# Performance work log

Measured on AMD Instinct MI355X. Metric: run time of the kernel, lower is better.

The kernel has to match this reference:

```python
import jax, jax.numpy as jnp
import numpy as np

# dims: B batches, N points/batch, S sampled points/batch, M image-projected points/batch,
# V voxels, (H,Wd) range-image size, HID hidden size, NSC scales, NCLS classes
B, N, S, M, V, H, Wd, HID, NSC, NCLS = 2, 120000, 40000, 30000, 100000, 256, 1024, 128, 4, 20


def setup_inputs() -> dict:
    key = jax.random.key(0)
    ks = jax.random.split(key, 24)
    f = jnp.float32
    w = lambda k, shp: (0.02 * jax.random.normal(k, shp, f))
    rows = jax.random.randint(ks[10], (B, M), 0, H, jnp.int32)
    cols = jax.random.randint(ks[11], (B, M), 0, Wd, jnp.int32)
    return {
        "pts_feat_layers": jax.random.normal(ks[0], (NSC, V, HID), f),
        "pts_sample_feat": jax.random.normal(ks[1], (NSC, B * S, HID), f),
        "img_latent_full": jax.random.normal(ks[2], (B, HID, H, Wd), f),
        "img_feat_layers": jax.random.normal(ks[3], (NSC, B * M, HID), f),
        "leaner_W": w(ks[4], (NSC, HID, HID)), "leaner_b": jnp.zeros((NSC, HID), f),
        "fcs1_W": w(ks[5], (NSC, 2 * HID, HID)), "fcs1_b": jnp.zeros((NSC, HID), f),
        "fcs2_W": w(ks[6], (NSC, HID, HID)), "fcs2_b": jnp.zeros((NSC, HID), f),
        "cls_W1": w(ks[7], (NSC * HID, 128)), "cls_b1": jnp.zeros((128,), f),
        "cls_W2": w(ks[8], (128, NCLS)), "cls_b2": jnp.zeros((NCLS,), f),
        "points_img": jnp.stack([rows, cols], axis=-1),              # [B,M,2]
        "point2img_index": jax.random.randint(ks[12], (B, M), 0, N, jnp.int32),
        "sample_index": jax.random.randint(ks[13], (B, S), 0, N, jnp.int32),
        "coors_inv": jax.random.randint(ks[14], (B * N,), 0, V, jnp.int32),
    }


def reference(pts_feat_layers, pts_sample_feat, img_latent_full, img_feat_layers,
              leaner_W, leaner_b, fcs1_W, fcs1_b, fcs2_W, fcs2_b,
              cls_W1, cls_b1, cls_W2, cls_b2,
              points_img, point2img_index, sample_index, coors_inv):
    dt = img_latent_full.dtype
    img_hw = jnp.transpose(img_latent_full, (0, 2, 3, 1))  # [B,H,Wd,HID]
    bar = jnp.arange(B)[:, None]
    # gather image features at projected pixel coords: [B,M,HID]
    img_at_pts = img_hw[bar, points_img[:, :, 0], points_img[:, :, 1]]
    # scatter image features to per-point slots (pts_img_batch_new): [B,N,HID]
    pimg = jax.vmap(lambda idx, v: jnp.zeros((N, HID), dt).at[idx].set(v))(point2img_index, img_at_pts)

    fuse_feats, enc_feats = [], []
    for i in range(NSC):
        # p2img_mapping_spsample: output values depend only on sampled feats + image gather
        sf = pts_sample_feat[i].reshape(B, S, HID)
        sp = jax.vmap(lambda idx, v: jnp.zeros((N, HID), dt).at[idx].set(v))(sample_index, sf)
        sp = sp + pimg  # sample_point_feat == sample_point_feat_f  [B,N,HID]
        # scatter fused point features back into voxel features, then gather per point
        pts_feat = pts_feat_layers[i].at[coors_inv].set(sp.reshape(B * N, HID))
        pts_point = pts_feat[coors_inv].reshape(B, N, HID)
        # p2img_mapping: gather the image-projected points per batch  [B*M,HID]
        pts_g = jnp.take_along_axis(pts_point, point2img_index[:, :, None], axis=1).reshape(B * M, HID)
        fl = jax.nn.relu(pts_g @ leaner_W[i] + leaner_b[i])
        fc = jnp.concatenate([img_feat_layers[i], fl], axis=1) @ fcs1_W[i] + fcs1_b[i]
        fw = jax.nn.sigmoid(fc @ fcs2_W[i] + fcs2_b[i])
        fuse_feats.append(jax.nn.relu(fc * fw))
        enc_feats.append(sp.reshape(B * N, HID))

    seg = jnp.concatenate(fuse_feats, axis=1)                       # [B*M, NSC*HID]
    img_seg_logits = jax.nn.relu(seg @ cls_W1 + cls_b1) @ cls_W2 + cls_b2  # [B*M, NCLS]
    output_3d = jnp.concatenate(enc_feats, axis=1)                  # [B*N, NSC*HID]
    return img_seg_logits, output_3d
```

## Files before the change

kernel.cpp:

```cpp
#include <hip/hip_runtime.h>
#include <hip/hip_bf16.h>
#include <math.h>

#define B_    2
#define N_    120000
#define S_    40000
#define M_    30000
#define V_    100000
#define H_    256
#define WD_   1024
#define HID_  128
#define NSC_  4
#define NCLS_ 20
#define BM_   60000
#define BS_   80000
#define BN_   240000

#define SCALE_BLKS 3752
#define OUT3D_BLKS 30000

typedef __attribute__((ext_vector_type(8))) short bfrag8;
typedef __attribute__((ext_vector_type(4))) float facc4;
typedef __attribute__((ext_vector_type(4))) unsigned short usvec4;

__device__ __forceinline__ unsigned short f2bf(float f){
  unsigned u = __builtin_bit_cast(unsigned, f);
  u += 0x7fffu + ((u >> 16) & 1u);
  return (unsigned short)(u >> 16);
}
__device__ __forceinline__ float bf2f(unsigned short s){
  return __builtin_bit_cast(float, ((unsigned)s) << 16);
}

__global__ __launch_bounds__(256) void k_front(
    const float* __restrict__ img, const int* __restrict__ ptsimg,
    unsigned short* __restrict__ iap,
    const int* __restrict__ p2i, const int* __restrict__ si,
    const int* __restrict__ ci,
    int* __restrict__ win_p, int* __restrict__ win_s, int* __restrict__ win_c,
    const float* __restrict__ lW, const float* __restrict__ f1W,
    const float* __restrict__ f2W, const float* __restrict__ c1W,
    const float* __restrict__ c2W,
    unsigned short* __restrict__ lwT, unsigned short* __restrict__ f1T,
    unsigned short* __restrict__ f2T, unsigned short* __restrict__ c1T,
    unsigned short* __restrict__ c2T){
  int bid = blockIdx.x;
  if (bid < 30000){
    int t = bid * 256 + threadIdx.x;
    int row = t >> 7, h = t & 127;
    int b = row / M_;
    int r = ptsimg[row * 2 + 0];
    int c = ptsimg[row * 2 + 1];
    iap[t] = f2bf(img[(((size_t)b * HID_ + h) * H_ + r) * WD_ + c]);
    return;
  }
  if (bid < 30938){
    int t = (bid - 30000) * 256 + threadIdx.x;
    if (t < BM_) atomicMax(&win_p[(t / M_) * N_ + p2i[t]], t);
    if (t < BS_) atomicMax(&win_s[(t / S_) * N_ + si[t]], t);
    if (t < BN_) atomicMax(&win_c[ci[t]], t);
    return;
  }
  {
    int t = (bid - 30938) * 256 + threadIdx.x;
    if (t < 65536){
      int i = t >> 14, r = t & 16383, n = r >> 7, k = r & 127;
      lwT[i * 16384 + n * 128 + k] = f2bf(lW[i * 16384 + k * 128 + n]);
    } else if (t < 196608){
      int e = t - 65536;
      int i = e >> 15, r = e & 32767, n = r >> 8, k = r & 255;
      f1T[i * 32768 + n * 256 + k] = f2bf(f1W[i * 32768 + k * 128 + n]);
    } else if (t < 262144){
      int e = t - 196608;
      int i = e >> 14, r = e & 16383, n = r >> 7, k = r & 127;
      f2T[i * 16384 + n * 128 + k] = f2bf(f2W[i * 16384 + k * 128 + n]);
    } else if (t < 327680){
      int e = t - 262144;
      int n = e >> 9, k = e & 511;
      c1T[n * 512 + k] = f2bf(c1W[k * 128 + n]);
    } else if (t < 330240){
      int e = t - 327680;
      int n = e >> 7, k = e & 127;
      c2T[n * 128 + k] = f2bf(c2W[k * NCLS_ + n]);
    }
    return;
  }
}

__global__ __launch_bounds__(256, 3) void k_mega(
    const float* __restrict__ samp, const unsigned short* __restrict__ iap,
    const int* __restrict__ win_p, const int* __restrict__ win_s,
    const int* __restrict__ win_c, const int* __restrict__ p2i,
    const int* __restrict__ ci, const float* __restrict__ imgf,
    const unsigned short* __restrict__ lwT, const float* __restrict__ lb,
    const unsigned short* __restrict__ f1T, const float* __restrict__ f1b,
    const unsigned short* __restrict__ f2T, const float* __restrict__ f2b,
    unsigned short* __restrict__ seg, float* __restrict__ o3d){
  __shared__ char lds[49152];
  if (blockIdx.x >= SCALE_BLKS){
    int t = (blockIdx.x - SCALE_BLKS) * 256 + threadIdx.x;
    int j = t >> 5, q = t & 31;
    int sj = win_s[j], pj = win_p[j];
    facc4 iv = {0.f, 0.f, 0.f, 0.f};
    if (pj >= 0){
      usvec4 u = __builtin_nontemporal_load((const usvec4*)(iap + (size_t)pj * HID_ + q * 4));
      iv.x = bf2f(u.x); iv.y = bf2f(u.y); iv.z = bf2f(u.z); iv.w = bf2f(u.w);
    }
    #pragma unroll
    for (int i = 0; i < NSC_; i++){
      facc4 v = iv;
      if (sj >= 0){
        facc4 s = __builtin_nontemporal_load((const facc4*)(samp + ((size_t)i * BS_ + sj) * HID_ + q * 4));
        v += s;
      }
      __builtin_nontemporal_store(v, (facc4*)(o3d + (size_t)j * (NSC_ * HID_) + i * HID_ + q * 4));
    }
    return;
  }
  char* actL = lds + 32768;
  const int i  = blockIdx.x & 3;
  const int rb = blockIdx.x >> 2;
  const int lane = threadIdx.x & 63, wv = threadIdx.x >> 6;
  const int rl = lane & 15, kg = lane >> 4;
  const int rowBase = rb * 64 + wv * 16;
  const int row = rowBase + rl;
  const bool rv = row < BM_;
  const int lr = wv * 16 + rl;

  {
    const char* src = (const char*)(lwT + (size_t)i * 16384);
    for (int c = threadIdx.x; c < 2048; c += 256){
      int byte = c << 4; int n = byte >> 8;
      *(bfrag8*)(lds + (byte ^ ((n & 7) << 4))) = *(const bfrag8*)(src + byte);
    }
  }
  bfrag8 afr[4];
  {
    int g = 0;
    if (rv){ int b = row >= M_; g = win_c[ci[b * N_ + p2i[row]]]; }
    int sj = rv ? win_s[g] : -1;
    int pj = rv ? win_p[g] : -1;
    const float* sp = samp + ((size_t)i * BS_ + (sj < 0 ? 0 : sj)) * HID_;
    const unsigned short* pp = iap + (size_t)(pj < 0 ? 0 : pj) * HID_;
    #pragma unroll
    for (int kc = 0; kc < 4; kc++){
      int k0 = kc * 32 + kg * 8;
      facc4 s0 = {0,0,0,0}, s1 = {0,0,0,0};
      if (sj >= 0){ s0 = *(const facc4*)(sp + k0); s1 = *(const facc4*)(sp + k0 + 4); }
      float g0=0,g1=0,g2=0,g3=0,g4=0,g5=0,g6=0,g7=0;
      if (pj >= 0){
        usvec4 u0 = *(const usvec4*)(pp + k0);
        usvec4 u1 = *(const usvec4*)(pp + k0 + 4);
        g0=bf2f(u0.x); g1=bf2f(u0.y); g2=bf2f(u0.z); g3=bf2f(u0.w);
        g4=bf2f(u1.x); g5=bf2f(u1.y); g6=bf2f(u1.z); g7=bf2f(u1.w);
      }
      bfrag8 a;
      a[0]=(short)f2bf(s0.x+g0); a[1]=(short)f2bf(s0.y+g1);
      a[2]=(short)f2bf(s0.z+g2); a[3]=(short)f2bf(s0.w+g3);
      a[4]=(short)f2bf(s1.x+g4); a[5]=(short)f2bf(s1.y+g5);
      a[6]=(short)f2bf(s1.z+g6); a[7]=(short)f2bf(s1.w+g7);
      afr[kc] = a;
    }
  }
  __syncthreads();
  facc4 accL[8];
  #pragma unroll
  for (int ct = 0; ct < 8; ct++) accL[ct] = (facc4){0.f,0.f,0.f,0.f};
  #pragma unroll
  for (int kc = 0; kc < 4; kc++){
    int k0 = kc * 32 + kg * 8;
    #pragma unroll
    for (int ct = 0; ct < 8; ct++){
      int col = ct * 16 + rl;
      int byte = (col << 8) + (k0 << 1);
      bfrag8 b = *(const bfrag8*)(lds + (byte ^ ((col & 7) << 4)));
      accL[ct] = __builtin_amdgcn_mfma_f32_16x16x32_bf16(afr[kc], b, accL[ct], 0, 0, 0);
    }
  }
  __syncthreads();
  {
    const float* bias = lb + i * HID_;
    #pragma unroll
    for (int ct = 0; ct < 8; ct++){
      int col = ct * 16 + rl;
      float bv = bias[col];
      #pragma unroll
      for (int r = 0; r < 4; r++){
        int ar = wv * 16 + kg * 4 + r;
        float v = accL[ct][r] + bv; v = v > 0.f ? v : 0.f;
        int byte = ar * 256 + col * 2;
        *(unsigned short*)(actL + (byte ^ ((ar & 7) << 4))) = f2bf(v);
      }
    }
    const char* src = (const char*)(f1T + (size_t)i * 32768);
    for (int c = threadIdx.x; c < 2048; c += 256){
      int n = c >> 4, off = (c & 15) << 4;
      *(bfrag8*)(lds + ((n * 256 + off) ^ ((n & 7) << 4))) =
          *(const bfrag8*)(src + (size_t)n * 512 + off);
    }
  }
  __syncthreads();
  facc4 accF[8];
  #pragma unroll
  for (int ct = 0; ct < 8; ct++) accF[ct] = (facc4){0.f,0.f,0.f,0.f};
  {
    const float* a1 = imgf + ((size_t)i * BM_ + (rv ? row : 0)) * HID_;
    #pragma unroll
    for (int kc = 0; kc < 4; kc++){
      int kk = kc * 32 + kg * 8;
      bfrag8 a = (bfrag8){0,0,0,0,0,0,0,0};
      if (rv){
        facc4 s0 = *(const facc4*)(a1 + kk);
        facc4 s1 = *(const facc4*)(a1 + kk + 4);
        a[0]=(short)f2bf(s0.x); a[1]=(short)f2bf(s0.y); a[2]=(short)f2bf(s0.z); a[3]=(short)f2bf(s0.w);
        a[4]=(short)f2bf(s1.x); a[5]=(short)f2bf(s1.y); a[6]=(short)f2bf(s1.z); a[7]=(short)f2bf(s1.w);
      }
      #pragma unroll
      for (int ct = 0; ct < 8; ct++){
        int col = ct * 16 + rl;
        int byte = (col << 8) + (kk << 1);
        bfrag8 b = *(const bfrag8*)(lds + (byte ^ ((col & 7) << 4)));
        accF[ct] = __builtin_amdgcn_mfma_f32_16x16x32_bf16(a, b, accF[ct], 0, 0, 0);
      }
    }
  }
  __syncthreads();
  {
    const char* src = (const char*)(f1T + (size_t)i * 32768) + 256;
    for (int c = threadIdx.x; c < 2048; c += 256){
      int n = c >> 4, off = (c & 15) << 4;
      *(bfrag8*)(lds + ((n * 256 + off) ^ ((n & 7) << 4))) =
          *(const bfrag8*)(src + (size_t)n * 512 + off);
    }
  }
  __syncthreads();
  #pragma unroll
  for (int kc = 0; kc < 4; kc++){
    int kl = kc * 32 + kg * 8;
    int byteA = lr * 256 + kl * 2;
    bfrag8 a = *(const bfrag8*)(actL + (byteA ^ ((lr & 7) << 4)));
    #pragma unroll
    for (int ct = 0; ct < 8; ct++){
      int col = ct * 16 + rl;
      int byte = (col << 8) + (kl << 1);
      bfrag8 b = *(const bfrag8*)(lds + (byte ^ ((col & 7) << 4)));
      accF[ct] = __builtin_amdgcn_mfma_f32_16x16x32_bf16(a, b, accF[ct], 0, 0, 0);
    }
  }
  __syncthreads();
  {
    const float* bias = f1b + i * HID_;
    #pragma unroll
    for (int ct = 0; ct < 8; ct++){
      int col = ct * 16 + rl;
      float bv = bias[col];
      #pragma unroll
      for (int r = 0; r < 4; r++){
        int ar = wv * 16 + kg * 4 + r;
        float v = accF[ct][r] + bv;
        accF[ct][r] = v;
        int byte = ar * 256 + col * 2;
        *(unsigned short*)(actL + (byte ^ ((ar & 7) << 4))) = f2bf(v);
      }
    }
    const char* src = (const char*)(f2T + (size_t)i * 16384);
    for (int c = threadIdx.x; c < 2048; c += 256){
      int byte = c << 4; int n = byte >> 8;
      *(bfrag8*)(lds + (byte ^ ((n & 7) << 4))) = *(const bfrag8*)(src + byte);
    }
  }
  __syncthreads();
  facc4 accT[8];
  #pragma unroll
  for (int ct = 0; ct < 8; ct++) accT[ct] = (facc4){0.f,0.f,0.f,0.f};
  #pragma unroll
  for (int kc = 0; kc < 4; kc++){
    int kk = kc * 32 + kg * 8;
    int byteA = lr * 256 + kk * 2;
    bfrag8 a = *(const bfrag8*)(actL + (byteA ^ ((lr & 7) << 4)));
    #pragma unroll
    for (int ct = 0; ct < 8; ct++){
      int col = ct * 16 + rl;
      int byte = (col << 8) + (kk << 1);
      bfrag8 b = *(const bfrag8*)(lds + (byte ^ ((col & 7) << 4)));
      accT[ct] = __builtin_amdgcn_mfma_f32_16x16x32_bf16(a, b, accT[ct], 0, 0, 0);
    }
  }
  {
    const float* bias2 = f2b + i * HID_;
    #pragma unroll
    for (int ct = 0; ct < 8; ct++){
      int col = ct * 16 + rl;
      float bv2 = bias2[col];
      #pragma unroll
      for (int r = 0; r < 4; r++){
        int orow = rowBase + kg * 4 + r;
        if (orow < BM_){
          float tv = accT[ct][r] + bv2;
          float fw = 1.f / (1.f + expf(-tv));
          float u = accF[ct][r] * fw;
          u = u > 0.f ? u : 0.f;
          seg[(size_t)orow * (NSC_ * HID_) + i * HID_ + col] = f2bf(u);
        }
      }
    }
  }
}

__global__ __launch_bounds__(256, 3) void k_cls(const unsigned short* __restrict__ seg,
    const unsigned short* __restrict__ c1T, const float* __restrict__ c1b,
    const unsigned short* __restrict__ c2T, const float* __restrict__ c2b,
    float* __restrict__ logits){
  __shared__ char lds[49152];
  char* actL = lds + 32768;
  const int lane = threadIdx.x & 63, wv = threadIdx.x >> 6;
  const int rl = lane & 15, kg = lane >> 4;
  const int rowBase = blockIdx.x * 64 + wv * 16;
  const int row = rowBase + rl;
  const bool rv = row < BM_;
  const unsigned short* ar = seg + (size_t)(rv ? row : 0) * 512;
  facc4 acc[8];
  #pragma unroll
  for (int ct = 0; ct < 8; ct++) acc[ct] = (facc4){0.f,0.f,0.f,0.f};
  for (int ph = 0; ph < 4; ph++){
    if (ph) __syncthreads();
    for (int c = threadIdx.x; c < 2048; c += 256){
      int n = c >> 4, off = (c & 15) << 4;
      *(bfrag8*)(lds + ((n * 256 + off) ^ ((n & 7) << 4))) =
          *(const bfrag8*)((const char*)c1T + (size_t)n * 1024 + ph * 256 + off);
    }
    __syncthreads();
    #pragma unroll
    for (int kc = 0; kc < 4; kc++){
      int kl = kc * 32 + kg * 8;
      bfrag8 a = (bfrag8){0,0,0,0,0,0,0,0};
      if (rv) a = *(const bfrag8*)(ar + ph * 128 + kl);
      #pragma unroll
      for (int ct = 0; ct < 8; ct++){
        int col = ct * 16 + rl;
        int byte = (col << 8) + (kl << 1);
        bfrag8 b = *(const bfrag8*)(lds + (byte ^ ((col & 7) << 4)));
        acc[ct] = __builtin_amdgcn_mfma_f32_16x16x32_bf16(a, b, acc[ct], 0, 0, 0);
      }
    }
  }
  __syncthreads();
  #pragma unroll
  for (int ct = 0; ct < 8; ct++){
    int col = ct * 16 + rl;
    float bv = c1b[col];
    #pragma unroll
    for (int r = 0; r < 4; r++){
      int arr = wv * 16 + kg * 4 + r;
      float v = acc[ct][r] + bv; v = v > 0.f ? v : 0.f;
      int byte = arr * 256 + col * 2;
      *(unsigned short*)(actL + (byte ^ ((arr & 7) << 4))) = f2bf(v);
    }
  }
  for (int c = threadIdx.x; c < 320; c += 256)
    *(bfrag8*)(lds + (c << 4)) = *(const bfrag8*)((const char*)c2T + (c << 4));
  __syncthreads();
  {
    int t = threadIdx.x;
    int lrd = t >> 2, n0 = (t & 3) * 5;
    int orow = blockIdx.x * 64 + lrd;
    if (orow < BM_){
      float accD[5];
      #pragma unroll
      for (int q = 0; q < 5; q++) accD[q] = c2b[n0 + q];
      #pragma unroll
      for (int k8 = 0; k8 < 16; k8++){
        int byteA = lrd * 256 + (k8 << 4);
        bfrag8 hv = *(const bfrag8*)(actL + (byteA ^ ((lrd & 7) << 4)));
        #pragma unroll
        for (int q = 0; q < 5; q++){
          bfrag8 w8 = *(const bfrag8*)(lds + (n0 + q) * 256 + (k8 << 4));
          #pragma unroll
          for (int e = 0; e < 8; e++)
            accD[q] += bf2f((unsigned short)hv[e]) * bf2f((unsigned short)w8[e]);
        }
      }
      #pragma unroll
      for (int q = 0; q < 5; q++)
        logits[(size_t)orow * NCLS_ + n0 + q] = accD[q];
    }
  }
}

extern "C" void kernel_launch(void* const* d_in, const int* in_sizes, int n_in,
                              void* d_out, int out_size, void* d_ws, size_t ws_size,
                              hipStream_t stream){
  const float* samp = (const float*)d_in[1];
  const float* img  = (const float*)d_in[2];
  const float* imgf = (const float*)d_in[3];
  const float* lW   = (const float*)d_in[4];
  const float* lb   = (const float*)d_in[5];
  const float* f1W  = (const float*)d_in[6];
  const float* f1b  = (const float*)d_in[7];
  const float* f2W  = (const float*)d_in[8];
  const float* f2b  = (const float*)d_in[9];
  const float* c1W  = (const float*)d_in[10];
  const float* c1b  = (const float*)d_in[11];
  const float* c2W  = (const float*)d_in[12];
  const float* c2b  = (const float*)d_in[13];
  const int* ptsimg = (const int*)d_in[14];
  const int* p2i    = (const int*)d_in[15];
  const int* si     = (const int*)d_in[16];
  const int* ci     = (const int*)d_in[17];

  char* ws = (char*)d_ws;
  int*   win_p = (int*)(ws + 0);
  int*   win_s = (int*)(ws + 960000);
  int*   win_c = (int*)(ws + 1920000);
  unsigned short* iap = (unsigned short*)(ws + 2320128);
  unsigned short* seg = (unsigned short*)(ws + 17680384);
  unsigned short* lwT = (unsigned short*)(ws + 79120512);
  unsigned short* f1T = lwT + 65536;
  unsigned short* f2T = f1T + 131072;
  unsigned short* c1T = f2T + 65536;
  unsigned short* c2T = c1T + 65536;

  float* logits = (float*)d_out;
  float* o3d    = (float*)d_out + (size_t)BM_ * NCLS_;

  (void)hipMemsetAsync(ws, 0xFF, 2320000, stream);
  k_front<<<32228, 256, 0, stream>>>(img, ptsimg, iap, p2i, si, ci,
                                     win_p, win_s, win_c,
                                     lW, f1W, f2W, c1W, c2W,
                                     lwT, f1T, f2T, c1T, c2T);
  k_mega <<<SCALE_BLKS + OUT3D_BLKS, 256, 0, stream>>>(samp, iap,
                                     win_p, win_s, win_c, p2i, ci, imgf,
                                     lwT, lb, f1T, f1b, f2T, f2b, seg, o3d);
  k_cls  <<<938, 256, 0, stream>>>(seg, c1T, c1b, c2T, c2b, logits);
}
```

Before: 489.7 us.

## Split o3d writer into own kernel and vectorize image gather per thread

```diff
diff --git a/kernel.cpp b/kernel.cpp
--- a/kernel.cpp
+++ b/kernel.cpp
@@ -16,9 +16,6 @@
 #define BS_   80000
 #define BN_   240000
 
-#define SCALE_BLKS 3752
-#define OUT3D_BLKS 30000
-
 typedef __attribute__((ext_vector_type(8))) short bfrag8;
 typedef __attribute__((ext_vector_type(4))) float facc4;
 typedef __attribute__((ext_vector_type(4))) unsigned short usvec4;
@@ -45,24 +42,15 @@
     unsigned short* __restrict__ f2T, unsigned short* __restrict__ c1T,
     unsigned short* __restrict__ c2T){
   int bid = blockIdx.x;
-  if (bid < 30000){
+  if (bid < 938){
     int t = bid * 256 + threadIdx.x;
-    int row = t >> 7, h = t & 127;
-    int b = row / M_;
-    int r = ptsimg[row * 2 + 0];
-    int c = ptsimg[row * 2 + 1];
-    iap[t] = f2bf(img[(((size_t)b * HID_ + h) * H_ + r) * WD_ + c]);
-    return;
-  }
-  if (bid < 30938){
-    int t = (bid - 30000) * 256 + threadIdx.x;
     if (t < BM_) atomicMax(&win_p[(t / M_) * N_ + p2i[t]], t);
     if (t < BS_) atomicMax(&win_s[(t / S_) * N_ + si[t]], t);
     if (t < BN_) atomicMax(&win_c[ci[t]], t);
     return;
   }
-  {
-    int t = (bid - 30938) * 256 + threadIdx.x;
+  if (bid < 2228){
+    int t = (bid - 938) * 256 + threadIdx.x;
     if (t < 65536){
       int i = t >> 14, r = t & 16383, n = r >> 7, k = r & 127;
       lwT[i * 16384 + n * 128 + k] = f2bf(lW[i * 16384 + k * 128 + n]);
@@ -85,9 +73,44 @@
     }
     return;
   }
-}
-
-__global__ __launch_bounds__(256, 3) void k_mega(
+  {
+    int t = (bid - 2228) * 256 + threadIdx.x;
+    int row = t >> 5, h4 = (t & 31) * 4;
+    int b = row / M_;
+    int r = ptsimg[row * 2 + 0];
+    int c = ptsimg[row * 2 + 1];
+    const float* base = img + (((size_t)b * HID_ + h4) * H_ + r) * WD_ + c;
+    const size_t st = (size_t)H_ * WD_;
+    float v0 = base[0], v1 = base[st], v2 = base[2 * st], v3 = base[3 * st];
+    usvec4 o = {f2bf(v0), f2bf(v1), f2bf(v2), f2bf(v3)};
+    *(usvec4*)(iap + (size_t)row * HID_ + h4) = o;
+    return;
+  }
+}
+
+__global__ __launch_bounds__(256) void k_o3d(const float* __restrict__ samp,
+    const int* __restrict__ win_s, const int* __restrict__ win_p,
+    const unsigned short* __restrict__ iap, float* __restrict__ o3d){
+  int t = blockIdx.x * 256 + threadIdx.x;
+  int j = t >> 5, q = t & 31;
+  int sj = win_s[j], pj = win_p[j];
+  facc4 iv = {0.f, 0.f, 0.f, 0.f};
+  if (pj >= 0){
+    usvec4 u = *(const usvec4*)(iap + (size_t)pj * HID_ + q * 4);
+    iv.x = bf2f(u.x); iv.y = bf2f(u.y); iv.z = bf2f(u.z); iv.w = bf2f(u.w);
+  }
+  #pragma unroll
+  for (int i = 0; i < NSC_; i++){
+    facc4 v = iv;
+    if (sj >= 0){
+      facc4 s = *(const facc4*)(samp + ((size_t)i * BS_ + sj) * HID_ + q * 4);
+      v += s;
+    }
+    __builtin_nontemporal_store(v, (facc4*)(o3d + (size_t)j * (NSC_ * HID_) + i * HID_ + q * 4));
+  }
+}
+
+__global__ __launch_bounds__(256, 3) void k_scales(
     const float* __restrict__ samp, const unsigned short* __restrict__ iap,
     const int* __restrict__ win_p, const int* __restrict__ win_s,
     const int* __restrict__ win_c, const int* __restrict__ p2i,
@@ -95,28 +118,8 @@
     const unsigned short* __restrict__ lwT, const float* __restrict__ lb,
     const unsigned short* __restrict__ f1T, const float* __restrict__ f1b,
     const unsigned short* __restrict__ f2T, const float* __restrict__ f2b,
-    unsigned short* __restrict__ seg, float* __restrict__ o3d){
+    unsigned short* __restrict__ seg){
   __shared__ char lds[49152];
-  if (blockIdx.x >= SCALE_BLKS){
-    int t = (blockIdx.x - SCALE_BLKS) * 256 + threadIdx.x;
-    int j = t >> 5, q = t & 31;
-    int sj = win_s[j], pj = win_p[j];
-    facc4 iv = {0.f, 0.f, 0.f, 0.f};
-    if (pj >= 0){
-      usvec4 u = __builtin_nontemporal_load((const usvec4*)(iap + (size_t)pj * HID_ + q * 4));
-      iv.x = bf2f(u.x); iv.y = bf2f(u.y); iv.z = bf2f(u.z); iv.w = bf2f(u.w);
-    }
-    #pragma unroll
-    for (int i = 0; i < NSC_; i++){
-      facc4 v = iv;
-      if (sj >= 0){
-        facc4 s = __builtin_nontemporal_load((const facc4*)(samp + ((size_t)i * BS_ + sj) * HID_ + q * 4));
-        v += s;
-      }
-      __builtin_nontemporal_store(v, (facc4*)(o3d + (size_t)j * (NSC_ * HID_) + i * HID_ + q * 4));
-    }
-    return;
-  }
   char* actL = lds + 32768;
   const int i  = blockIdx.x & 3;
   const int rb = blockIdx.x >> 2;
@@ -424,12 +427,12 @@
   float* o3d    = (float*)d_out + (size_t)BM_ * NCLS_;
 
   (void)hipMemsetAsync(ws, 0xFF, 2320000, stream);
-  k_front<<<32228, 256, 0, stream>>>(img, ptsimg, iap, p2i, si, ci,
-                                     win_p, win_s, win_c,
-                                     lW, f1W, f2W, c1W, c2W,
-                                     lwT, f1T, f2T, c1T, c2T);
-  k_mega <<<SCALE_BLKS + OUT3D_BLKS, 256, 0, stream>>>(samp, iap,
-                                     win_p, win_s, win_c, p2i, ci, imgf,
-                                     lwT, lb, f1T, f1b, f2T, f2b, seg, o3d);
-  k_cls  <<<938, 256, 0, stream>>>(seg, c1T, c1b, c2T, c2b, logits);
-}
+  k_front  <<<9728,  256, 0, stream>>>(img, ptsimg, iap, p2i, si, ci,
+                                       win_p, win_s, win_c,
+                                       lW, f1W, f2W, c1W, c2W,
+                                       lwT, f1T, f2T, c1T, c2T);
+  k_o3d    <<<30000, 256, 0, stream>>>(samp, win_s, win_p, iap, o3d);
+  k_scales <<<3752,  256, 0, stream>>>(samp, iap, win_p, win_s, win_c, p2i, ci,
+                                       imgf, lwT, lb, f1T, f1b, f2T, f2b, seg);
+  k_cls    <<<938,   256, 0, stream>>>(seg, c1T, c1b, c2T, c2b, logits);
+}
```

Result: faster. 459.9 us (-6.1%).
